# Optimization experiments

Measured on AMD Instinct MI355X. Metric: run time of the kernel, lower is better.

The kernel has to match this reference:

```python
import jax, jax.numpy as jnp
import numpy as np

N, E, D, K = 50000, 800000, 128, 128


def _graph_conv(x, src, dst, w, W_rel, b_rel, W_root, n_nodes):
    # PyG GraphConv (aggr='add'): out = lin_rel(sum_j w_ij * x_j) + lin_root(x)
    msg = w[:, None] * x[src]                              # [E, D]
    agg = jax.ops.segment_sum(msg, dst, num_segments=n_nodes)  # [N, D]
    return agg @ W_rel + b_rel + x @ W_root


def setup_inputs() -> dict:
    key = jax.random.key(0)
    ks = jax.random.split(key, 16)
    sc = 1.0 / np.sqrt(D).astype(np.float32)
    inp = {
        "x": jax.random.normal(ks[0], (N, D), dtype=jnp.float32),
        "edge_index": jax.random.randint(ks[1], (2, E), 0, N, dtype=jnp.int64 if jax.config.jax_enable_x64 else jnp.int32),
        "edge_weight": jax.random.uniform(ks[2], (E,), dtype=jnp.float32),
        # GraphConv layer 1
        "W_rel1": jax.random.normal(ks[3], (D, D), dtype=jnp.float32) * sc,
        "b_rel1": jnp.zeros((D,), dtype=jnp.float32),
        "W_root1": jax.random.normal(ks[4], (D, D), dtype=jnp.float32) * sc,
        # GraphConv layer 2
        "W_rel2": jax.random.normal(ks[5], (D, D), dtype=jnp.float32) * sc,
        "b_rel2": jnp.zeros((D,), dtype=jnp.float32),
        "W_root2": jax.random.normal(ks[6], (D, D), dtype=jnp.float32) * sc,
        # MLP: Linear(D,128) + Identity, then final Linear(128,K)
        "W_m1": jax.random.normal(ks[7], (D, 128), dtype=jnp.float32) * sc,
        "b_m1": jnp.zeros((128,), dtype=jnp.float32),
        "W_out": jax.random.normal(ks[8], (128, K), dtype=jnp.float32) * (1.0 / np.sqrt(128).astype(np.float32)),
        "b_out": jnp.zeros((K,), dtype=jnp.float32),
    }
    return inp


def reference(x, edge_index, edge_weight, W_rel1, b_rel1, W_root1,
              W_rel2, b_rel2, W_root2, W_m1, b_m1, W_out, b_out):
    n_nodes = x.shape[0]
    src, dst = edge_index[0], edge_index[1]

    # Message passing stack with ReLU
    h = jax.nn.relu(_graph_conv(x, src, dst, edge_weight, W_rel1, b_rel1, W_root1, n_nodes))
    h = jax.nn.relu(_graph_conv(h, src, dst, edge_weight, W_rel2, b_rel2, W_root2, n_nodes))

    # MLP -> cluster logits (mlp_act = Identity)
    s = (h @ W_m1 + b_m1) @ W_out + b_out                  # [N, K]
    probs = jax.nn.softmax(s, axis=-1)                     # [N, K]

    # dense_mincut_pool losses (computed edge-wise; A = to_dense_adj(edge_index, w))
    # degree d_i = sum_j A[i, j] = scatter of w over src
    deg = jax.ops.segment_sum(edge_weight, src, num_segments=n_nodes)  # [N]
    # mincut_num = trace(S^T A S) = sum_e w_e * <S[src_e], S[dst_e]>
    mincut_num = jnp.einsum('e,ek,ek->', edge_weight, probs[src], probs[dst])
    # mincut_den = trace(S^T D S) = sum_i d_i * ||S_i||^2
    mincut_den = jnp.sum(deg * jnp.sum(probs * probs, axis=-1))
    mc_loss = -(mincut_num / mincut_den)

    # orthogonality loss: || SS/||SS||_F - I/sqrt(K) ||_F
    ss = probs.T @ probs                                   # [K, K]
    k = probs.shape[1]
    o_loss = jnp.linalg.norm(ss / jnp.linalg.norm(ss) - jnp.eye(k, dtype=ss.dtype) / np.float32(np.sqrt(k)))

    return probs, mc_loss, o_loss
```

## Files before the change

### kernel.cpp

```cpp
#include <hip/hip_runtime.h>
#include <hip/hip_bf16.h>

#define D 128
#define KT 32
#define SS_BLOCKS 256

__global__ __launch_bounds__(256) void hist_deg_kernel(const int* __restrict__ src,
                                                       const int* __restrict__ dst,
                                                       const float* __restrict__ w,
                                                       int* __restrict__ cnt,
                                                       float* __restrict__ deg, int E) {
    int e = blockIdx.x * 256 + threadIdx.x;
    if (e < E) {
        atomicAdd(&cnt[dst[e]], 1);
        atomicAdd(&deg[src[e]], w[e]);
    }
}

__global__ __launch_bounds__(256) void scan_chunk_kernel(const int* __restrict__ cnt,
                                                         int* __restrict__ rowptr,
                                                         int* __restrict__ aux, int N) {
    __shared__ int ts[256];
    int t = threadIdx.x;
    int base = blockIdx.x * 1024 + t * 4;
    int v[4], s = 0;
#pragma unroll
    for (int i = 0; i < 4; ++i) {
        v[i] = (base + i < N) ? cnt[base + i] : 0;
        s += v[i];
    }
    ts[t] = s;
    __syncthreads();
#pragma unroll
    for (int off = 1; off < 256; off <<= 1) {
        int add = (t >= off) ? ts[t - off] : 0;
        __syncthreads();
        ts[t] += add;
        __syncthreads();
    }
    int run = ts[t] - s;
#pragma unroll
    for (int i = 0; i < 4; ++i) {
        run += v[i];
        if (base + i < N) rowptr[base + i + 1] = run;
    }
    if (t == 255) aux[blockIdx.x] = ts[255];
}

__global__ void scan_aux_kernel(int* __restrict__ aux, int nb) {
    if (threadIdx.x == 0) {
        int s = 0;
        for (int i = 0; i < nb; ++i) { s += aux[i]; aux[i] = s; }
    }
}

__global__ __launch_bounds__(256) void add_off_kernel(int* __restrict__ rowptr,
                                                      const int* __restrict__ aux, int N) {
    int i = blockIdx.x * 256 + threadIdx.x;
    if (i == 0) rowptr[0] = 0;
    if (i < N) {
        int b = i >> 10;
        if (b > 0) rowptr[i + 1] += aux[b - 1];
    }
}

__global__ __launch_bounds__(256) void fill_kernel(const int* __restrict__ src,
                                                   const int* __restrict__ dst,
                                                   const float* __restrict__ w,
                                                   const int* __restrict__ rowptr,
                                                   int* __restrict__ cur,
                                                   int* __restrict__ csr_src,
                                                   float* __restrict__ csr_w, int E) {
    int e = blockIdx.x * 256 + threadIdx.x;
    if (e < E) {
        int d = dst[e];
        int pos = rowptr[d] + atomicAdd(&cur[d], 1);
        csr_src[pos] = src[e];
        csr_w[pos] = w[e];
    }
}

#define ACC4(acc, we, v) { acc.x += (we) * (v).x; acc.y += (we) * (v).y; \
                           acc.z += (we) * (v).z; acc.w += (we) * (v).w; }

__global__ __launch_bounds__(256) void gather_kernel(const float* __restrict__ xin,
                                                     const int* __restrict__ csr_src,
                                                     const float* __restrict__ csr_w,
                                                     const int* __restrict__ rowptr,
                                                     float* __restrict__ agg, int N) {
    int node = blockIdx.x * 4 + (threadIdx.x >> 6);
    if (node >= N) return;
    int lane = threadIdx.x & 63;
    int half = lane >> 5;
    int c4 = (lane & 31) * 4;
    int beg = rowptr[node], end = rowptr[node + 1];
    float4 a0 = make_float4(0.f, 0.f, 0.f, 0.f);
    float4 a1 = make_float4(0.f, 0.f, 0.f, 0.f);
    int j = beg;
    for (; j + 3 < end; j += 4) {
        int e0 = j + half, e1 = j + 2 + half;
        int s0 = csr_src[e0]; float w0 = csr_w[e0];
        int s1 = csr_src[e1]; float w1 = csr_w[e1];
        float4 v0 = *(const float4*)&xin[(size_t)s0 * D + c4];
        float4 v1 = *(const float4*)&xin[(size_t)s1 * D + c4];
        ACC4(a0, w0, v0);
        ACC4(a1, w1, v1);
    }
    if (j + 1 < end) {
        int e0 = j + half;
        int s0 = csr_src[e0]; float w0 = csr_w[e0];
        float4 v0 = *(const float4*)&xin[(size_t)s0 * D + c4];
        ACC4(a0, w0, v0);
        j += 2;
    }
    if (j < end && half == 0) {
        int s0 = csr_src[j]; float w0 = csr_w[j];
        float4 v0 = *(const float4*)&xin[(size_t)s0 * D + c4];
        ACC4(a0, w0, v0);
    }
    a0.x += a1.x; a0.y += a1.y; a0.z += a1.z; a0.w += a1.w;
    a0.x += __shfl_xor(a0.x, 32);
    a0.y += __shfl_xor(a0.y, 32);
    a0.z += __shfl_xor(a0.z, 32);
    a0.w += __shfl_xor(a0.w, 32);
    if (half == 0) *(float4*)&agg[(size_t)node * D + c4] = a0;
}

#define FMA4(acc, a, wv) { acc.x += (a) * (wv).x; acc.y += (a) * (wv).y; \
                           acc.z += (a) * (wv).z; acc.w += (a) * (wv).w; }

__global__ __launch_bounds__(256) void lin_kernel(const float* __restrict__ A1,
                                                  const float* __restrict__ A2,
                                                  const float* __restrict__ W1,
                                                  const float* __restrict__ W2,
                                                  const float* __restrict__ b,
                                                  float* __restrict__ out, int N) {
    __shared__ float As[KT][132];
    __shared__ float Ws[KT][D];
    int tid = threadIdx.x;
    int r0 = blockIdx.x * 128;
    int ty4 = (tid >> 3) * 4;
    int tx16 = (tid & 7) * 16;

    float4 acc[4][4];
#pragma unroll
    for (int i = 0; i < 4; ++i)
#pragma unroll
        for (int j = 0; j < 4; ++j) acc[i][j] = make_float4(0.f, 0.f, 0.f, 0.f);

    for (int t = 0; t < 8; ++t) {
        const float* A = (t < 4) ? A1 : A2;
        const float* W = (t < 4) ? W1 : W2;
        int koff = (t & 3) * KT;
        __syncthreads();
#pragma unroll
        for (int i = 0; i < 4; ++i) {
            int f4 = tid + i * 256;
            int row = f4 >> 3;
            int c4 = f4 & 7;
            float4 v = make_float4(0.f, 0.f, 0.f, 0.f);
            if (r0 + row < N) v = *(const float4*)&A[(size_t)(r0 + row) * D + koff + c4 * 4];
            As[c4 * 4 + 0][row] = v.x;
            As[c4 * 4 + 1][row] = v.y;
            As[c4 * 4 + 2][row] = v.z;
            As[c4 * 4 + 3][row] = v.w;
        }
#pragma unroll
        for (int i = 0; i < 4; ++i) {
            int f4 = tid + i * 256;
            int k = f4 >> 5;
            int c4 = f4 & 31;
            *(float4*)&Ws[k][c4 * 4] = *(const float4*)&W[(size_t)(koff + k) * D + c4 * 4];
        }
        __syncthreads();
#pragma unroll 4
        for (int k = 0; k < KT; ++k) {
            float4 av = *(const float4*)&As[k][ty4];
            float4 w0 = *(const float4*)&Ws[k][tx16];
            float4 w1 = *(const float4*)&Ws[k][tx16 + 4];
            float4 w2 = *(const float4*)&Ws[k][tx16 + 8];
            float4 w3 = *(const float4*)&Ws[k][tx16 + 12];
            FMA4(acc[0][0], av.x, w0); FMA4(acc[0][1], av.x, w1);
            FMA4(acc[0][2], av.x, w2); FMA4(acc[0][3], av.x, w3);
            FMA4(acc[1][0], av.y, w0); FMA4(acc[1][1], av.y, w1);
            FMA4(acc[1][2], av.y, w2); FMA4(acc[1][3], av.y, w3);
            FMA4(acc[2][0], av.z, w0); FMA4(acc[2][1], av.z, w1);
            FMA4(acc[2][2], av.z, w2); FMA4(acc[2][3], av.z, w3);
            FMA4(acc[3][0], av.w, w0); FMA4(acc[3][1], av.w, w1);
            FMA4(acc[3][2], av.w, w2); FMA4(acc[3][3], av.w, w3);
        }
    }
    float4 bv[4];
#pragma unroll
    for (int j = 0; j < 4; ++j) bv[j] = *(const float4*)&b[tx16 + j * 4];
#pragma unroll
    for (int i = 0; i < 4; ++i) {
        int r = r0 + ty4 + i;
        if (r < N) {
#pragma unroll
            for (int j = 0; j < 4; ++j) {
                float4 v;
                v.x = fmaxf(acc[i][j].x + bv[j].x, 0.f);
                v.y = fmaxf(acc[i][j].y + bv[j].y, 0.f);
                v.z = fmaxf(acc[i][j].z + bv[j].z, 0.f);
                v.w = fmaxf(acc[i][j].w + bv[j].w, 0.f);
                *(float4*)&out[(size_t)r * D + tx16 + j * 4] = v;
            }
        }
    }
}

__global__ __launch_bounds__(256) void smallmm_kernel(const float* __restrict__ Wm1,
                                                      const float* __restrict__ bm1,
                                                      const float* __restrict__ Wout,
                                                      const float* __restrict__ bout,
                                                      float* __restrict__ Wc,
                                                      float* __restrict__ bc) {
    int idx = blockIdx.x * 256 + threadIdx.x;
    if (blockIdx.x < 64) {
        int i = idx >> 7, j = idx & 127;
        float s = 0.f;
        for (int k = 0; k < 128; ++k) s += Wm1[i * 128 + k] * Wout[k * 128 + j];
        Wc[idx] = s;
    } else {
        int j = threadIdx.x;
        if (j < 128) {
            float s = bout[j];
            for (int k = 0; k < 128; ++k) s += bm1[k] * Wout[k * 128 + j];
            bc[j] = s;
        }
    }
}

__global__ __launch_bounds__(256) void out_softmax_kernel(const float* __restrict__ h2,
                                                          const float* __restrict__ Wc,
                                                          const float* __restrict__ bc,
                                                          const float* __restrict__ deg,
                                                          float* __restrict__ probs,
                                                          float* __restrict__ accum, int N) {
    __shared__ float Rs[32][128];
    __shared__ float Ws[128 * 64];
    int tid = threadIdx.x;
    int wave = tid >> 6, lane = tid & 63;
    int r0 = blockIdx.x * 32;
#pragma unroll
    for (int i = 0; i < 4; ++i) {
        int f4 = tid + i * 256;
        int row = f4 >> 5;
        int c4 = f4 & 31;
        float4 v = make_float4(0.f, 0.f, 0.f, 0.f);
        if (r0 + row < N) v = *(const float4*)&h2[(size_t)(r0 + row) * D + c4 * 4];
        *(float4*)&Rs[row][c4 * 4] = v;
    }
    float lg[8][2];
#pragma unroll
    for (int h = 0; h < 2; ++h) {
        __syncthreads();
#pragma unroll
        for (int i = 0; i < 8; ++i) {
            int f4 = tid + i * 256;
            int k = f4 >> 4;
            int c4 = f4 & 15;
            *(float4*)&Ws[k * 64 + c4 * 4] = *(const float4*)&Wc[(size_t)k * 128 + h * 64 + c4 * 4];
        }
        __syncthreads();
        float bv = bc[h * 64 + lane];
        float a[8];
#pragma unroll
        for (int ri = 0; ri < 8; ++ri) a[ri] = bv;
        for (int k = 0; k < 128; ++k) {
            float wv = Ws[k * 64 + lane];
#pragma unroll
            for (int ri = 0; ri < 8; ++ri) a[ri] += Rs[wave + ri * 4][k] * wv;
        }
#pragma unroll
        for (int ri = 0; ri < 8; ++ri) lg[ri][h] = a[ri];
    }
    float den_local = 0.f;
#pragma unroll
    for (int ri = 0; ri < 8; ++ri) {
        int row = wave + ri * 4;
        int gr = r0 + row;
        float m = fmaxf(lg[ri][0], lg[ri][1]);
#pragma unroll
        for (int s = 32; s >= 1; s >>= 1) m = fmaxf(m, __shfl_xor(m, s));
        float e0 = expf(lg[ri][0] - m);
        float e1 = expf(lg[ri][1] - m);
        float sum = e0 + e1;
#pragma unroll
        for (int s = 32; s >= 1; s >>= 1) sum += __shfl_xor(sum, s);
        float inv = 1.f / sum;
        float p0 = e0 * inv, p1 = e1 * inv;
        float sq = p0 * p0 + p1 * p1;
#pragma unroll
        for (int s = 32; s >= 1; s >>= 1) sq += __shfl_xor(sq, s);
        if (gr < N) {
            probs[(size_t)gr * D + lane]      = p0;
            probs[(size_t)gr * D + 64 + lane] = p1;
            if (lane == 0) den_local += deg[gr] * sq;
        }
    }
    if (lane == 0 && den_local != 0.f) atomicAdd(&accum[1], den_local);
}

__global__ __launch_bounds__(256) void num_csr_kernel(const float* __restrict__ probs,
                                                      const int* __restrict__ csr_src,
                                                      const float* __restrict__ csr_w,
                                                      const int* __restrict__ rowptr,
                                                      float* __restrict__ accum, int N) {
    int tid = threadIdx.x;
    int wave = tid >> 6, lane = tid & 63;
    int half = lane >> 5;
    int c4 = (lane & 31) * 4;
    float acc = 0.f;
    int stride = gridDim.x * 4;
    for (int node = blockIdx.x * 4 + wave; node < N; node += stride) {
        float4 pd = *(const float4*)&probs[(size_t)node * D + c4];
        int beg = rowptr[node], end = rowptr[node + 1];
        int j = beg;
        for (; j + 3 < end; j += 4) {
            int e0 = j + half, e1 = j + 2 + half;
            int s0 = csr_src[e0]; float w0 = csr_w[e0];
            int s1 = csr_src[e1]; float w1 = csr_w[e1];
            float4 p0 = *(const float4*)&probs[(size_t)s0 * D + c4];
            float4 p1 = *(const float4*)&probs[(size_t)s1 * D + c4];
            acc += w0 * (p0.x * pd.x + p0.y * pd.y + p0.z * pd.z + p0.w * pd.w)
                 + w1 * (p1.x * pd.x + p1.y * pd.y + p1.z * pd.z + p1.w * pd.w);
        }
        if (j + 1 < end) {
            int e0 = j + half;
            int s0 = csr_src[e0]; float w0 = csr_w[e0];
            float4 p0 = *(const float4*)&probs[(size_t)s0 * D + c4];
            acc += w0 * (p0.x * pd.x + p0.y * pd.y + p0.z * pd.z + p0.w * pd.w);
            j += 2;
        }
        if (j < end && half == 0) {
            int s0 = csr_src[j]; float w0 = csr_w[j];
            float4 p0 = *(const float4*)&probs[(size_t)s0 * D + c4];
            acc += w0 * (p0.x * pd.x + p0.y * pd.y + p0.z * pd.z + p0.w * pd.w);
        }
    }
#pragma unroll
    for (int m = 32; m >= 1; m >>= 1) acc += __shfl_xor(acc, m);
    if (lane == 0 && acc != 0.f) atomicAdd(&accum[0], acc);
}

__global__ __launch_bounds__(256) void ss_kernel(const float* __restrict__ probs,
                                                 float* __restrict__ partial, int N) {
    __shared__ float Ps[32][132];
    int tid = threadIdx.x;
    int a0 = (tid >> 4) * 8;
    int b0 = (tid & 15) * 8;
    float acc[8][8];
#pragma unroll
    for (int i = 0; i < 8; ++i)
#pragma unroll
        for (int j = 0; j < 8; ++j) acc[i][j] = 0.f;

    int rowsPerBlk = (N + gridDim.x - 1) / gridDim.x;
    int rbeg = blockIdx.x * rowsPerBlk;
    int rend = rbeg + rowsPerBlk;
    if (rend > N) rend = N;

    for (int c = rbeg; c < rend; c += 32) {
        int nr = rend - c;
        if (nr > 32) nr = 32;
        __syncthreads();
        for (int i = tid; i < nr * 32; i += 256) {
            int r = i >> 5, c4 = i & 31;
            *(float4*)&Ps[r][c4 * 4] = *(const float4*)&probs[(size_t)(c + r) * D + c4 * 4];
        }
        __syncthreads();
        for (int r = 0; r < nr; ++r) {
            float4 av0 = *(const float4*)&Ps[r][a0];
            float4 av1 = *(const float4*)&Ps[r][a0 + 4];
            float4 bv0 = *(const float4*)&Ps[r][b0];
            float4 bv1 = *(const float4*)&Ps[r][b0 + 4];
            float av[8] = {av0.x, av0.y, av0.z, av0.w, av1.x, av1.y, av1.z, av1.w};
            float bv[8] = {bv0.x, bv0.y, bv0.z, bv0.w, bv1.x, bv1.y, bv1.z, bv1.w};
#pragma unroll
            for (int i = 0; i < 8; ++i)
#pragma unroll
                for (int j = 0; j < 8; ++j) acc[i][j] += av[i] * bv[j];
        }
    }
    float* pb = partial + (size_t)blockIdx.x * 16384;
#pragma unroll
    for (int i = 0; i < 8; ++i) {
        *(float4*)&pb[(a0 + i) * 128 + b0]     = make_float4(acc[i][0], acc[i][1], acc[i][2], acc[i][3]);
        *(float4*)&pb[(a0 + i) * 128 + b0 + 4] = make_float4(acc[i][4], acc[i][5], acc[i][6], acc[i][7]);
    }
}

__global__ __launch_bounds__(256) void ss_reduce_kernel(const float* __restrict__ partial,
                                                        float* __restrict__ ss) {
    int i = blockIdx.x * 256 + threadIdx.x;
    float s = 0.f;
    for (int b = 0; b < SS_BLOCKS; ++b) s += partial[(size_t)b * 16384 + i];
    ss[i] = s;
}

__global__ __launch_bounds__(256) void finalize_kernel(const float* __restrict__ ss,
                                                       const float* __restrict__ accum,
                                                       float* __restrict__ out2) {
    int tid = threadIdx.x;
    __shared__ float wsum[4], wsum2[4];
    float s = 0.f;
    for (int i = tid; i < 16384; i += 256) { float v = ss[i]; s += v * v; }
#pragma unroll
    for (int m = 32; m >= 1; m >>= 1) s += __shfl_xor(s, m);
    if ((tid & 63) == 0) wsum[tid >> 6] = s;
    __syncthreads();
    float norm = sqrtf(wsum[0] + wsum[1] + wsum[2] + wsum[3]);
    float inv = 1.f / norm;
    const float rk = 0.08838834764831845f;
    float o = 0.f;
    for (int i = tid; i < 16384; i += 256) {
        int a = i >> 7, b = i & 127;
        float v = ss[i] * inv - (a == b ? rk : 0.f);
        o += v * v;
    }
#pragma unroll
    for (int m = 32; m >= 1; m >>= 1) o += __shfl_xor(o, m);
    if ((tid & 63) == 0) wsum2[tid >> 6] = o;
    __syncthreads();
    if (tid == 0) {
        out2[0] = -(accum[0] / accum[1]);
        out2[1] = sqrtf(wsum2[0] + wsum2[1] + wsum2[2] + wsum2[3]);
    }
}

extern "C" void kernel_launch(void* const* d_in, const int* in_sizes, int n_in,
                              void* d_out, int out_size, void* d_ws, size_t ws_size,
                              hipStream_t stream) {
    const float* x      = (const float*)d_in[0];
    const int*   ei     = (const int*)d_in[1];
    const float* w      = (const float*)d_in[2];
    const float* Wrel1  = (const float*)d_in[3];
    const float* brel1  = (const float*)d_in[4];
    const float* Wroot1 = (const float*)d_in[5];
    const float* Wrel2  = (const float*)d_in[6];
    const float* brel2  = (const float*)d_in[7];
    const float* Wroot2 = (const float*)d_in[8];
    const float* Wm1    = (const float*)d_in[9];
    const float* bm1    = (const float*)d_in[10];
    const float* Wout   = (const float*)d_in[11];
    const float* bout   = (const float*)d_in[12];

    int N = in_sizes[0] / D;
    int E = in_sizes[2];
    const int* src = ei;
    const int* dst = ei + E;

    float* probs = (float*)d_out;
    float* out2  = probs + (size_t)N * D;
    float* h2    = probs;

    float* ws    = (float*)d_ws;
    float* agg   = ws;
    float* h1    = ws + (size_t)N * D;
    float* Wc    = ws + (size_t)2 * N * D;
    float* bc    = Wc + 16384;
    float* ssb   = bc + 128;
    float* deg   = ssb + 16384;
    float* accum = deg + N;
    float* csr_w = accum + 2;
    int*   cnt   = (int*)(csr_w + E);
    int*   cur   = cnt + N;
    int*   rowptr= cur + N;
    int*   aux   = rowptr + N + 1;
    int*   csr_src = aux + 64;

    hipMemsetAsync(deg, 0, (size_t)(N + 2) * sizeof(float), stream);
    hipMemsetAsync(cnt, 0, (size_t)2 * N * sizeof(int), stream);

    int eGrid = (E + 255) / 256;
    int nb = (N + 1023) / 1024;
    int linGrid = (N + 127) / 128;
    int nodeGrid = (N + 3) / 4;

    hist_deg_kernel<<<eGrid, 256, 0, stream>>>(src, dst, w, cnt, deg, E);
    scan_chunk_kernel<<<nb, 256, 0, stream>>>(cnt, rowptr, aux, N);
    scan_aux_kernel<<<1, 64, 0, stream>>>(aux, nb);
    add_off_kernel<<<(N + 255) / 256, 256, 0, stream>>>(rowptr, aux, N);
    fill_kernel<<<eGrid, 256, 0, stream>>>(src, dst, w, rowptr, cur, csr_src, csr_w, E);

    gather_kernel<<<nodeGrid, 256, 0, stream>>>(x, csr_src, csr_w, rowptr, agg, N);
    lin_kernel<<<linGrid, 256, 0, stream>>>(agg, x, Wrel1, Wroot1, brel1, h1, N);
    gather_kernel<<<nodeGrid, 256, 0, stream>>>(h1, csr_src, csr_w, rowptr, agg, N);
    lin_kernel<<<linGrid, 256, 0, stream>>>(agg, h1, Wrel2, Wroot2, brel2, h2, N);
    smallmm_kernel<<<65, 256, 0, stream>>>(Wm1, bm1, Wout, bout, Wc, bc);
    out_softmax_kernel<<<(N + 31) / 32, 256, 0, stream>>>(h2, Wc, bc, deg, probs, accum, N);
    num_csr_kernel<<<2048, 256, 0, stream>>>(probs, csr_src, csr_w, rowptr, accum, N);
    ss_kernel<<<SS_BLOCKS, 256, 0, stream>>>(probs, agg, N);
    ss_reduce_kernel<<<64, 256, 0, stream>>>(agg, ssb);
    finalize_kernel<<<1, 256, 0, stream>>>(ssb, accum, out2);
}
```

Before: 728.6 us.

## Gather mincut-numerator neighbours from a bf16 probs copy; unroll edge loops deeper

```diff
diff --git a/kernel.cpp b/kernel.cpp
--- a/kernel.cpp
+++ b/kernel.cpp
@@ -4,6 +4,10 @@
 #define D 128
 #define KT 32
 #define SS_BLOCKS 256
+
+__device__ __forceinline__ float bf2f(unsigned short u) {
+    return __uint_as_float((unsigned)u << 16);
+}
 
 __global__ __launch_bounds__(256) void hist_deg_kernel(const int* __restrict__ src,
                                                        const int* __restrict__ dst,
@@ -96,29 +100,39 @@
     int beg = rowptr[node], end = rowptr[node + 1];
     float4 a0 = make_float4(0.f, 0.f, 0.f, 0.f);
     float4 a1 = make_float4(0.f, 0.f, 0.f, 0.f);
+    float4 a2 = make_float4(0.f, 0.f, 0.f, 0.f);
+    float4 a3 = make_float4(0.f, 0.f, 0.f, 0.f);
     int j = beg;
-    for (; j + 3 < end; j += 4) {
-        int e0 = j + half, e1 = j + 2 + half;
+    for (; j + 7 < end; j += 8) {
+        int e0 = j + half, e1 = j + 2 + half, e2 = j + 4 + half, e3 = j + 6 + half;
         int s0 = csr_src[e0]; float w0 = csr_w[e0];
         int s1 = csr_src[e1]; float w1 = csr_w[e1];
+        int s2 = csr_src[e2]; float w2 = csr_w[e2];
+        int s3 = csr_src[e3]; float w3 = csr_w[e3];
         float4 v0 = *(const float4*)&xin[(size_t)s0 * D + c4];
         float4 v1 = *(const float4*)&xin[(size_t)s1 * D + c4];
+        float4 v2 = *(const float4*)&xin[(size_t)s2 * D + c4];
+        float4 v3 = *(const float4*)&xin[(size_t)s3 * D + c4];
         ACC4(a0, w0, v0);
         ACC4(a1, w1, v1);
-    }
-    if (j + 1 < end) {
+        ACC4(a2, w2, v2);
+        ACC4(a3, w3, v3);
+    }
+    for (; j + 1 < end; j += 2) {
         int e0 = j + half;
         int s0 = csr_src[e0]; float w0 = csr_w[e0];
         float4 v0 = *(const float4*)&xin[(size_t)s0 * D + c4];
         ACC4(a0, w0, v0);
-        j += 2;
     }
     if (j < end && half == 0) {
         int s0 = csr_src[j]; float w0 = csr_w[j];
         float4 v0 = *(const float4*)&xin[(size_t)s0 * D + c4];
         ACC4(a0, w0, v0);
     }
-    a0.x += a1.x; a0.y += a1.y; a0.z += a1.z; a0.w += a1.w;
+    a0.x += a1.x + a2.x + a3.x;
+    a0.y += a1.y + a2.y + a3.y;
+    a0.z += a1.z + a2.z + a3.z;
+    a0.w += a1.w + a2.w + a3.w;
     a0.x += __shfl_xor(a0.x, 32);
     a0.y += __shfl_xor(a0.y, 32);
     a0.z += __shfl_xor(a0.z, 32);
@@ -237,6 +251,7 @@
                                                           const float* __restrict__ bc,
                                                           const float* __restrict__ deg,
                                                           float* __restrict__ probs,
+                                                          unsigned short* __restrict__ pbh,
                                                           float* __restrict__ accum, int N) {
     __shared__ float Rs[32][128];
     __shared__ float Ws[128 * 64];
@@ -297,6 +312,9 @@
         if (gr < N) {
             probs[(size_t)gr * D + lane]      = p0;
             probs[(size_t)gr * D + 64 + lane] = p1;
+            unsigned u0 = __float_as_uint(p0), u1 = __float_as_uint(p1);
+            pbh[(size_t)gr * D + lane]      = (unsigned short)((u0 + 0x8000u) >> 16);
+            pbh[(size_t)gr * D + 64 + lane] = (unsigned short)((u1 + 0x8000u) >> 16);
             if (lane == 0) den_local += deg[gr] * sq;
         }
     }
@@ -304,6 +322,7 @@
 }
 
 __global__ __launch_bounds__(256) void num_csr_kernel(const float* __restrict__ probs,
+                                                      const unsigned short* __restrict__ pbh,
                                                       const int* __restrict__ csr_src,
                                                       const float* __restrict__ csr_w,
                                                       const int* __restrict__ rowptr,
@@ -318,26 +337,31 @@
         float4 pd = *(const float4*)&probs[(size_t)node * D + c4];
         int beg = rowptr[node], end = rowptr[node + 1];
         int j = beg;
-        for (; j + 3 < end; j += 4) {
-            int e0 = j + half, e1 = j + 2 + half;
+        for (; j + 7 < end; j += 8) {
+            int e0 = j + half, e1 = j + 2 + half, e2 = j + 4 + half, e3 = j + 6 + half;
             int s0 = csr_src[e0]; float w0 = csr_w[e0];
             int s1 = csr_src[e1]; float w1 = csr_w[e1];
-            float4 p0 = *(const float4*)&probs[(size_t)s0 * D + c4];
-            float4 p1 = *(const float4*)&probs[(size_t)s1 * D + c4];
-            acc += w0 * (p0.x * pd.x + p0.y * pd.y + p0.z * pd.z + p0.w * pd.w)
-                 + w1 * (p1.x * pd.x + p1.y * pd.y + p1.z * pd.z + p1.w * pd.w);
-        }
-        if (j + 1 < end) {
+            int s2 = csr_src[e2]; float w2 = csr_w[e2];
+            int s3 = csr_src[e3]; float w3 = csr_w[e3];
+            ushort4 q0 = *(const ushort4*)&pbh[(size_t)s0 * D + c4];
+            ushort4 q1 = *(const ushort4*)&pbh[(size_t)s1 * D + c4];
+            ushort4 q2 = *(const ushort4*)&pbh[(size_t)s2 * D + c4];
+            ushort4 q3 = *(const ushort4*)&pbh[(size_t)s3 * D + c4];
+            acc += w0 * (bf2f(q0.x) * pd.x + bf2f(q0.y) * pd.y + bf2f(q0.z) * pd.z + bf2f(q0.w) * pd.w);
+            acc += w1 * (bf2f(q1.x) * pd.x + bf2f(q1.y) * pd.y + bf2f(q1.z) * pd.z + bf2f(q1.w) * pd.w);
+            acc += w2 * (bf2f(q2.x) * pd.x + bf2f(q2.y) * pd.y + bf2f(q2.z) * pd.z + bf2f(q2.w) * pd.w);
+            acc += w3 * (bf2f(q3.x) * pd.x + bf2f(q3.y) * pd.y + bf2f(q3.z) * pd.z + bf2f(q3.w) * pd.w);
+        }
+        for (; j + 1 < end; j += 2) {
             int e0 = j + half;
             int s0 = csr_src[e0]; float w0 = csr_w[e0];
-            float4 p0 = *(const float4*)&probs[(size_t)s0 * D + c4];
-            acc += w0 * (p0.x * pd.x + p0.y * pd.y + p0.z * pd.z + p0.w * pd.w);
-            j += 2;
+            ushort4 q0 = *(const ushort4*)&pbh[(size_t)s0 * D + c4];
+            acc += w0 * (bf2f(q0.x) * pd.x + bf2f(q0.y) * pd.y + bf2f(q0.z) * pd.z + bf2f(q0.w) * pd.w);
         }
         if (j < end && half == 0) {
             int s0 = csr_src[j]; float w0 = csr_w[j];
-            float4 p0 = *(const float4*)&probs[(size_t)s0 * D + c4];
-            acc += w0 * (p0.x * pd.x + p0.y * pd.y + p0.z * pd.z + p0.w * pd.w);
+            ushort4 q0 = *(const ushort4*)&pbh[(size_t)s0 * D + c4];
+            acc += w0 * (bf2f(q0.x) * pd.x + bf2f(q0.y) * pd.y + bf2f(q0.z) * pd.z + bf2f(q0.w) * pd.w);
         }
     }
 #pragma unroll
@@ -471,6 +495,8 @@
     int*   aux   = rowptr + N + 1;
     int*   csr_src = aux + 64;
 
+    unsigned short* pbh = (unsigned short*)h1;
+
     hipMemsetAsync(deg, 0, (size_t)(N + 2) * sizeof(float), stream);
     hipMemsetAsync(cnt, 0, (size_t)2 * N * sizeof(int), stream);
 
@@ -490,8 +516,8 @@
     gather_kernel<<<nodeGrid, 256, 0, stream>>>(h1, csr_src, csr_w, rowptr, agg, N);
     lin_kernel<<<linGrid, 256, 0, stream>>>(agg, h1, Wrel2, Wroot2, brel2, h2, N);
     smallmm_kernel<<<65, 256, 0, stream>>>(Wm1, bm1, Wout, bout, Wc, bc);
-    out_softmax_kernel<<<(N + 31) / 32, 256, 0, stream>>>(h2, Wc, bc, deg, probs, accum, N);
-    num_csr_kernel<<<2048, 256, 0, stream>>>(probs, csr_src, csr_w, rowptr, accum, N);
+    out_softmax_kernel<<<(N + 31) / 32, 256, 0, stream>>>(h2, Wc, bc, deg, probs, pbh, accum, N);
+    num_csr_kernel<<<2048, 256, 0, stream>>>(probs, pbh, csr_src, csr_w, rowptr, accum, N);
     ss_kernel<<<SS_BLOCKS, 256, 0, stream>>>(probs, agg, N);
     ss_reduce_kernel<<<64, 256, 0, stream>>>(agg, ssb);
     finalize_kernel<<<1, 256, 0, stream>>>(ssb, accum, out2);
```

Result: faster. 708.4 us (-2.8%).
